# Optimization experiments

Measured on AMD Instinct MI355X. Metric: run time of the kernel, lower is better.

## Reference

```python
import jax, jax.numpy as jnp
import numpy as np

T = 4.0
B = 8192
C = 1024
N_CLASSES = 100

def setup_inputs() -> dict:
    key = jax.random.key(0)
    k1, k2 = jax.random.split(key)
    output = jax.random.normal(k1, (B, C), dtype=jnp.float32)
    target = jax.random.randint(k2, (B,), 0, N_CLASSES, dtype=jnp.int64)
    return {"output": output, "target": target}

def reference(output, target):
    # Faithful to the torch module:
    #   probs = softmax(logits / T) + 1e-8   (the label_inds masking is dead code,
    #   probs is immediately overwritten in the original)
    #   kl[i, j] = F.kl_div(probs[i], probs[j])  with default reduction='mean'
    #            = mean_c( probs[j] * (log(probs[j]) - probs[i]) )
    #   (note: torch kl_div treats its first arg as LOG-probs, but the original
    #    passes raw probs -- we reproduce that exactly)
    #   loss = sum over same-label pairs (i != j) of kl[i,j]**2, divided by batch.
    n_cats = output.shape[1]
    probs = jax.nn.softmax(output / T, axis=1) + 1e-8          # [B, C]
    # self-term t[j] = mean_c probs[j] * log probs[j]
    t = jnp.mean(probs * jnp.log(probs), axis=1)               # [B]
    # cross[i, j] = mean_c probs[j] * probs[i]  (single big GEMM)
    cross = (probs @ probs.T) / n_cats                         # [B, B]
    kl = t[None, :] - cross                                    # kl[i, j]
    labels = target
    same = labels[:, None] == labels[None, :]                  # [B, B]
    not_diag = ~jnp.eye(labels.shape[0], dtype=bool)
    mask = (same & not_diag).astype(kl.dtype)
    # |kl|^2 summed over valid pairs; groups of size 1 contribute no pairs,
    # matching the original's `continue`.
    loss = jnp.sum(mask * kl * kl) / labels.shape[0]
    return loss
```

## Files before the change

kernel.cpp:

```cpp
#include <hip/hip_runtime.h>

#define B_SZ 8192
#define C_SZ 1024
#define NCLS 100
#define INV_T 0.25f
#define MAX_ITEMS 65536
#define GRP 64
#define NCH 8

typedef unsigned int uint32;

using bf16x8 = __attribute__((ext_vector_type(8))) short;
using f32x16 = __attribute__((ext_vector_type(16))) float;

__device__ __forceinline__ unsigned short f2bf(float f) {
    uint32 u = __float_as_uint(f);
    u = u + 0x7fffu + ((u >> 16) & 1u);
    return (unsigned short)(u >> 16);
}

__device__ __forceinline__ void gload16_lds(const void* g, void* l) {
    __builtin_amdgcn_global_load_lds(
        (const __attribute__((address_space(1))) uint32*)g,
        (__attribute__((address_space(3))) uint32*)l, 16, 0, 0);
}

__global__ __launch_bounds__(256) void softmax_prep_kernel(
        const float* __restrict__ x, const int* __restrict__ target,
        uint32* __restrict__ probs_bf, float* __restrict__ t,
        int* __restrict__ counts, int* __restrict__ lists,
        int* __restrict__ items, int* __restrict__ nitems,
        float* __restrict__ accum, int* __restrict__ done_ctr) {
    int tid = threadIdx.x;

    if (blockIdx.x == 0) {
        __shared__ int cnt[NCLS];
        __shared__ int tbase[NCLS];
        if (tid < NCLS) cnt[tid] = 0;
        if (tid == 0) { accum[0] = 0.0f; done_ctr[0] = 0; }
        __syncthreads();
        #pragma unroll 4
        for (int i = 0; i < B_SZ / 256; i++) {
            int r = i * 256 + tid;
            int lbl = target[r];
            if (lbl < 0) lbl = 0;
            if (lbl >= NCLS) lbl = NCLS - 1;
            int slot = atomicAdd(&cnt[lbl], 1);
            lists[lbl * B_SZ + slot] = r;
        }
        __syncthreads();
        if (tid < NCLS) counts[tid] = cnt[tid];
        if (tid == 0) {
            int tot = 0;
            for (int k = 0; k < NCLS; k++) {
                int ng = (cnt[k] + GRP - 1) / GRP;
                tbase[k] = tot;
                tot += ng * ng;
            }
            nitems[0] = tot;
        }
        __syncthreads();
        if (tid < NCLS) {
            int ng = (cnt[tid] + GRP - 1) / GRP;
            int base = tbase[tid];
            int z = 0;
            for (int a = 0; a < ng; a++)
                for (int b = 0; b < ng; b++)
                    items[base + z++] = tid | (a << 8) | (b << 20);
        }
        return;
    }

    int row = blockIdx.x - 1;
    const float4* xr = (const float4*)(x + (size_t)row * C_SZ);
    float4 v = xr[tid];
    v.x *= INV_T; v.y *= INV_T; v.z *= INV_T; v.w *= INV_T;

    __shared__ float red[12];
    int wid = tid >> 6;

    float m = fmaxf(fmaxf(v.x, v.y), fmaxf(v.z, v.w));
    #pragma unroll
    for (int o = 32; o >= 1; o >>= 1) m = fmaxf(m, __shfl_xor(m, o, 64));
    if ((tid & 63) == 0) red[wid] = m;
    __syncthreads();
    m = fmaxf(fmaxf(red[0], red[1]), fmaxf(red[2], red[3]));

    float4 e;
    e.x = __expf(v.x - m); e.y = __expf(v.y - m);
    e.z = __expf(v.z - m); e.w = __expf(v.w - m);
    float s = (e.x + e.y) + (e.z + e.w);
    #pragma unroll
    for (int o = 32; o >= 1; o >>= 1) s += __shfl_xor(s, o, 64);
    if ((tid & 63) == 0) red[4 + wid] = s;
    __syncthreads();
    float Z = (red[4] + red[5]) + (red[6] + red[7]);
    float rZ = 1.0f / Z;

    float4 p;
    p.x = e.x * rZ + 1e-8f; p.y = e.y * rZ + 1e-8f;
    p.z = e.z * rZ + 1e-8f; p.w = e.w * rZ + 1e-8f;

    uint2 packed;
    packed.x = ((uint32)f2bf(p.y) << 16) | (uint32)f2bf(p.x);
    packed.y = ((uint32)f2bf(p.w) << 16) | (uint32)f2bf(p.z);
    ((uint2*)(probs_bf + (size_t)row * (C_SZ / 2)))[tid] = packed;

    float pl = p.x * __logf(p.x) + p.y * __logf(p.y) +
               p.z * __logf(p.z) + p.w * __logf(p.w);
    #pragma unroll
    for (int o = 32; o >= 1; o >>= 1) pl += __shfl_xor(pl, o, 64);
    if ((tid & 63) == 0) red[8 + wid] = pl;
    __syncthreads();
    if (tid == 0)
        t[row] = ((red[8] + red[9]) + (red[10] + red[11])) * (1.0f / C_SZ);
}

__global__ __launch_bounds__(256, 1) void pair_kernel(
        const char* __restrict__ probs, const float* __restrict__ t,
        const int* __restrict__ counts, const int* __restrict__ lists,
        const int* __restrict__ nitems, const int* __restrict__ items,
        float* __restrict__ accum, int* __restrict__ done_ctr,
        float* __restrict__ out) {
    __shared__ uint32 sA[2 * GRP * 64];
    __shared__ uint32 sB[2 * GRP * 64];
    __shared__ int s_ridA[GRP];
    __shared__ int s_ridB[GRP];
    __shared__ float s_tB[GRP];
    __shared__ float s_wsum[4];

    int tid = threadIdx.x;
    int wv = tid >> 6;
    int lane = tid & 63;
    int l = lane & 31;
    int h = lane >> 5;
    int NI = nitems[0];
    if (NI > MAX_ITEMS) NI = MAX_ITEMS;
    float lacc = 0.0f;

    for (int it = blockIdx.x; it < NI; it += (int)gridDim.x) {
        int pk = items[it];
        int k = pk & 255;
        if (k >= NCLS) continue;
        int gi = (pk >> 8) & 0xfff;
        int gj = pk >> 20;
        int m = counts[k];
        if (m < 1) continue;
        if (m > B_SZ) m = B_SZ;
        bool same = (gi == gj);

        __syncthreads();
        if (tid < GRP) {
            int which = gi * GRP + tid; if (which > m - 1) which = m - 1;
            s_ridA[tid] = lists[k * B_SZ + which] & (B_SZ - 1);
        } else if (tid < 2 * GRP) {
            int r = tid - GRP;
            int which = gj * GRP + r; if (which > m - 1) which = m - 1;
            int rid = lists[k * B_SZ + which] & (B_SZ - 1);
            s_ridB[r] = rid;
            s_tB[r] = t[rid];
        }
        __syncthreads();

        int rowsA = m - gi * GRP; if (rowsA > GRP) rowsA = GRP;
        int rowsB = m - gj * GRP; if (rowsB > GRP) rowsB = GRP;
        int ntA = (rowsA + 31) >> 5;
        int ntB = (rowsB + 31) >> 5;
        int npairs = ntA * ntB;
        int ti = wv / ntB;
        int tj = wv % ntB;

        #define STAGE(ch, bb)                                                     \
            _Pragma("unroll")                                                     \
            for (int rr = 0; rr < 8; rr++) {                                      \
                if (!(same && rr >= 4)) {                                         \
                    int slot = rr * 256 + tid;                                    \
                    int row = (slot >> 4) & 63;                                   \
                    int c16 = slot & 15;                                          \
                    int rid = (rr >= 4) ? s_ridB[row] : s_ridA[row];              \
                    const char* gp = probs + ((size_t)rid << 11) + ((ch) << 8) +  \
                                     ((c16 ^ (row & 7)) << 4);                    \
                    uint32* lp = ((rr >= 4) ? sB : sA) + (bb) * (GRP * 64) +      \
                                 (((rr & 3) * 256 + wv * 64) << 2);               \
                    gload16_lds(gp, lp);                                          \
                }                                                                 \
            }

        STAGE(0, 0);
        __syncthreads();

        f32x16 acc = {};
        int bb = 0;
        #pragma unroll 1
        for (int ch = 0; ch < NCH; ch++) {
            if (ch + 1 < NCH) STAGE(ch + 1, bb ^ 1);
            if (wv < npairs) {
                const uint32* pA = sA + bb * (GRP * 64);
                const uint32* pB = (same ? sA : sB) + bb * (GRP * 64);
                #pragma unroll
                for (int ks = 0; ks < 8; ks++) {
                    int ra = ti * 32 + l;
                    int ca = (ks * 2 + h) ^ (ra & 7);
                    bf16x8 av = *(const bf16x8*)(pA + ra * 64 + ca * 4);
                    int rb = tj * 32 + l;
                    int cb = (ks * 2 + h) ^ (rb & 7);
                    bf16x8 bv = *(const bf16x8*)(pB + rb * 64 + cb * 4);
                    acc = __builtin_amdgcn_mfma_f32_32x32x16_bf16(av, bv, acc, 0, 0, 0);
                }
            }
            __syncthreads();
            bb ^= 1;
        }
        #undef STAGE

        if (wv < npairs) {
            int jloc = tj * 32 + l;
            int jl = gj * GRP + jloc;
            bool jv = jl < m;
            float tjv = s_tB[jloc];
            float local = 0.0f;
            #pragma unroll
            for (int g = 0; g < 16; g++) {
                int rowloc = (g & 3) + 8 * (g >> 2) + 4 * h;
                int il = gi * GRP + ti * 32 + rowloc;
                if (jv && il < m && il != jl) {
                    float kl = tjv - acc[g] * (1.0f / C_SZ);
                    local += kl * kl;
                }
            }
            lacc += local;
        }
    }

    #pragma unroll
    for (int o = 32; o >= 1; o >>= 1) lacc += __shfl_xor(lacc, o, 64);
    __syncthreads();
    if (lane == 0) s_wsum[wv] = lacc;
    __syncthreads();
    if (tid == 0) {
        float tot = (s_wsum[0] + s_wsum[1]) + (s_wsum[2] + s_wsum[3]);
        atomicAdd(accum, tot);
        __threadfence();
        if (atomicAdd(done_ctr, 1) == (int)gridDim.x - 1) {
            __threadfence();
            out[0] = atomicAdd(accum, 0.0f) * (1.0f / B_SZ);
        }
    }
}

extern "C" void kernel_launch(void* const* d_in, const int* in_sizes, int n_in,
                              void* d_out, int out_size, void* d_ws, size_t ws_size,
                              hipStream_t stream) {
    const float* x = (const float*)d_in[0];
    const int* target = (const int*)d_in[1];
    float* out = (float*)d_out;

    char* ws = (char*)d_ws;
    uint32* probs_bf = (uint32*)ws;
    char* p = ws + (size_t)B_SZ * C_SZ * 2;
    float* t = (float*)p;            p += B_SZ * 4;
    int* counts = (int*)p;           p += 128 * 4;
    int* nitems = (int*)p;           p += 16;
    int* lists = (int*)p;            p += (size_t)NCLS * B_SZ * 4;
    int* items = (int*)p;            p += MAX_ITEMS * 4;
    float* accum = (float*)p;        p += 16;
    int* done_ctr = (int*)p;

    softmax_prep_kernel<<<B_SZ + 1, 256, 0, stream>>>(x, target, probs_bf, t,
                                                      counts, lists, items, nitems,
                                                      accum, done_ctr);
    pair_kernel<<<512, 256, 0, stream>>>((const char*)probs_bf, t, counts, lists,
                                         nitems, items, accum, done_ctr, out);
}
```

Baseline: 104.4 us.

## Exploit pair symmetry with 128-row groups and upper-triangular tile scheduling

Class groups grow to 128 rows, and only upper-triangular group pairs and tile pairs are scheduled. Off-diagonal tiles add both kl[i,j]^2 and kl[j,i]^2 from one GEMM result, using t of both the row and the column, which roughly halves the MFMA and load work. Blocks become 512 threads with 8 waves, each wave owning up to two 32x32 tiles. The loop uses explicit vmcnt waits and raw barriers for double-buffered global-to-LDS loads, and the grid shrinks to 128 blocks, which risks load imbalance and fewer waves resident across CUs.

```diff
diff --git a/kernel.cpp b/kernel.cpp
--- a/kernel.cpp
+++ b/kernel.cpp
@@ -5,8 +5,9 @@
 #define NCLS 100
 #define INV_T 0.25f
 #define MAX_ITEMS 65536
-#define GRP 64
 #define NCH 8
+#define GRP 128
+#define PAIR_GRID 128
 
 typedef unsigned int uint32;
 
@@ -55,7 +56,7 @@
             for (int k = 0; k < NCLS; k++) {
                 int ng = (cnt[k] + GRP - 1) / GRP;
                 tbase[k] = tot;
-                tot += ng * ng;
+                tot += ng * (ng + 1) / 2;
             }
             nitems[0] = tot;
         }
@@ -65,7 +66,7 @@
             int base = tbase[tid];
             int z = 0;
             for (int a = 0; a < ng; a++)
-                for (int b = 0; b < ng; b++)
+                for (int b = a; b < ng; b++)
                     items[base + z++] = tid | (a << 8) | (b << 20);
         }
         return;
@@ -116,24 +117,24 @@
         t[row] = ((red[8] + red[9]) + (red[10] + red[11])) * (1.0f / C_SZ);
 }
 
-__global__ __launch_bounds__(256, 1) void pair_kernel(
+__global__ __launch_bounds__(512, 2) void pair_kernel(
         const char* __restrict__ probs, const float* __restrict__ t,
         const int* __restrict__ counts, const int* __restrict__ lists,
         const int* __restrict__ nitems, const int* __restrict__ items,
         float* __restrict__ accum, int* __restrict__ done_ctr,
         float* __restrict__ out) {
-    __shared__ uint32 sA[2 * GRP * 64];
-    __shared__ uint32 sB[2 * GRP * 64];
+    __shared__ char sAB[2][2][32768];
     __shared__ int s_ridA[GRP];
     __shared__ int s_ridB[GRP];
+    __shared__ float s_tA[GRP];
     __shared__ float s_tB[GRP];
-    __shared__ float s_wsum[4];
+    __shared__ float s_wsum[8];
 
     int tid = threadIdx.x;
     int wv = tid >> 6;
-    int lane = tid & 63;
-    int l = lane & 31;
-    int h = lane >> 5;
+    int ln = tid & 63;
+    int l = ln & 31;
+    int h = ln >> 5;
     int NI = nitems[0];
     if (NI > MAX_ITEMS) NI = MAX_ITEMS;
     float lacc = 0.0f;
@@ -147,18 +148,20 @@
         int m = counts[k];
         if (m < 1) continue;
         if (m > B_SZ) m = B_SZ;
-        bool same = (gi == gj);
+        bool same_strip = (gi == gj);
 
         __syncthreads();
         if (tid < GRP) {
             int which = gi * GRP + tid; if (which > m - 1) which = m - 1;
-            s_ridA[tid] = lists[k * B_SZ + which] & (B_SZ - 1);
+            int r = lists[k * B_SZ + which] & (B_SZ - 1);
+            s_ridA[tid] = r;
+            s_tA[tid] = t[r];
         } else if (tid < 2 * GRP) {
-            int r = tid - GRP;
-            int which = gj * GRP + r; if (which > m - 1) which = m - 1;
-            int rid = lists[k * B_SZ + which] & (B_SZ - 1);
-            s_ridB[r] = rid;
-            s_tB[r] = t[rid];
+            int rb = tid - GRP;
+            int which = gj * GRP + rb; if (which > m - 1) which = m - 1;
+            int r = lists[k * B_SZ + which] & (B_SZ - 1);
+            s_ridB[rb] = r;
+            s_tB[rb] = t[r];
         }
         __syncthreads();
 
@@ -166,79 +169,145 @@
         int rowsB = m - gj * GRP; if (rowsB > GRP) rowsB = GRP;
         int ntA = (rowsA + 31) >> 5;
         int ntB = (rowsB + 31) >> 5;
-        int npairs = ntA * ntB;
-        int ti = wv / ntB;
-        int tj = wv % ntB;
-
-        #define STAGE(ch, bb)                                                     \
-            _Pragma("unroll")                                                     \
-            for (int rr = 0; rr < 8; rr++) {                                      \
-                if (!(same && rr >= 4)) {                                         \
-                    int slot = rr * 256 + tid;                                    \
-                    int row = (slot >> 4) & 63;                                   \
-                    int c16 = slot & 15;                                          \
-                    int rid = (rr >= 4) ? s_ridB[row] : s_ridA[row];              \
-                    const char* gp = probs + ((size_t)rid << 11) + ((ch) << 8) +  \
-                                     ((c16 ^ (row & 7)) << 4);                    \
-                    uint32* lp = ((rr >= 4) ? sB : sA) + (bb) * (GRP * 64) +      \
-                                 (((rr & 3) * 256 + wv * 64) << 2);               \
-                    gload16_lds(gp, lp);                                          \
-                }                                                                 \
-            }
-
-        STAGE(0, 0);
-        __syncthreads();
-
-        f32x16 acc = {};
-        int bb = 0;
-        #pragma unroll 1
-        for (int ch = 0; ch < NCH; ch++) {
-            if (ch + 1 < NCH) STAGE(ch + 1, bb ^ 1);
-            if (wv < npairs) {
-                const uint32* pA = sA + bb * (GRP * 64);
-                const uint32* pB = (same ? sA : sB) + bb * (GRP * 64);
+
+        int P = same_strip ? (ntA * (ntA + 1)) / 2 : ntA * ntB;
+        int tta[2], ttb[2], pv[2];
+        #pragma unroll
+        for (int slot = 0; slot < 2; slot++) {
+            int p = wv + slot * 8;
+            pv[slot] = (p < P);
+            int pp = pv[slot] ? p : 0;
+            int a = 0, b = 0;
+            if (same_strip) {
+                int rem = pp, len = ntA;
+                while (rem >= len) { rem -= len; a++; len--; }
+                b = a + rem;
+            } else {
+                a = pp / ntB; b = pp % ntB;
+            }
+            tta[slot] = a; ttb[slot] = b;
+        }
+
+        const char* gA[4];
+        const char* gB[4];
+        #pragma unroll
+        for (int s = 0; s < 4; s++) {
+            int row = s * 32 + wv * 4 + (ln >> 4);
+            int c16 = ln & 15;
+            int off = ((c16 ^ (row & 7)) << 4);
+            gA[s] = probs + ((size_t)s_ridA[row] << 11) + off;
+            gB[s] = probs + ((size_t)s_ridB[row] << 11) + off;
+        }
+
+        #define STAGE_A(ch, db)                                                \
+            _Pragma("unroll")                                                  \
+            for (int s = 0; s < 4; s++)                                        \
+                gload16_lds(gA[s] + ((ch) << 8), &sAB[db][0][s * 8192 + wv * 1024]);
+        #define STAGE_B(ch, db)                                                \
+            _Pragma("unroll")                                                  \
+            for (int s = 0; s < 4; s++)                                        \
+                gload16_lds(gB[s] + ((ch) << 8), &sAB[db][1][s * 8192 + wv * 1024]);
+
+        #define COMPUTE(db, bs)                                                \
+            { const char* bufA_ = &sAB[db][0][0];                              \
+              const char* bufB_ = &sAB[db][bs][0];                             \
+              _Pragma("unroll")                                                \
+              for (int slot = 0; slot < 2; slot++) {                           \
+                  if (pv[slot]) {                                              \
+                      _Pragma("unroll")                                        \
+                      for (int ks = 0; ks < 4; ks++) {                         \
+                          int ca = ((2 * ks + h) ^ (l & 7)) << 4;              \
+                          bf16x8 av = *(const bf16x8*)(bufA_ + (tta[slot] * 32 + l) * 256 + ca); \
+                          bf16x8 bv = *(const bf16x8*)(bufB_ + (ttb[slot] * 32 + l) * 256 + ca); \
+                          acc[slot] = __builtin_amdgcn_mfma_f32_32x32x16_bf16(av, bv, acc[slot], 0, 0, 0); \
+                      }                                                        \
+                  }                                                            \
+              } }
+
+        f32x16 acc[2] = {};
+        if (same_strip) {
+            STAGE_A(0, 0);
+            #pragma unroll 1
+            for (int ch = 0; ch < NCH; ch++) {
+                int db = ch & 1;
+                if (ch + 1 < NCH) {
+                    STAGE_A(ch + 1, db ^ 1);
+                    asm volatile("s_waitcnt vmcnt(4)" ::: "memory");
+                } else {
+                    asm volatile("s_waitcnt vmcnt(0)" ::: "memory");
+                }
+                __builtin_amdgcn_sched_barrier(0);
+                __builtin_amdgcn_s_barrier();
+                __builtin_amdgcn_sched_barrier(0);
+                COMPUTE(db, 0);
+                __builtin_amdgcn_sched_barrier(0);
+                __builtin_amdgcn_s_barrier();
+            }
+        } else {
+            STAGE_A(0, 0); STAGE_B(0, 0);
+            #pragma unroll 1
+            for (int ch = 0; ch < NCH; ch++) {
+                int db = ch & 1;
+                if (ch + 1 < NCH) {
+                    STAGE_A(ch + 1, db ^ 1); STAGE_B(ch + 1, db ^ 1);
+                    asm volatile("s_waitcnt vmcnt(8)" ::: "memory");
+                } else {
+                    asm volatile("s_waitcnt vmcnt(0)" ::: "memory");
+                }
+                __builtin_amdgcn_sched_barrier(0);
+                __builtin_amdgcn_s_barrier();
+                __builtin_amdgcn_sched_barrier(0);
+                COMPUTE(db, 1);
+                __builtin_amdgcn_sched_barrier(0);
+                __builtin_amdgcn_s_barrier();
+            }
+        }
+        #undef STAGE_A
+        #undef STAGE_B
+        #undef COMPUTE
+
+        float local = 0.0f;
+        #pragma unroll
+        for (int slot = 0; slot < 2; slot++) {
+            if (pv[slot]) {
+                bool dtile = same_strip && (tta[slot] == ttb[slot]);
+                int jloc = ttb[slot] * 32 + l;
+                int jl = gj * GRP + jloc;
+                bool jv = jl < m;
+                float tcol = s_tB[jloc];
                 #pragma unroll
-                for (int ks = 0; ks < 8; ks++) {
-                    int ra = ti * 32 + l;
-                    int ca = (ks * 2 + h) ^ (ra & 7);
-                    bf16x8 av = *(const bf16x8*)(pA + ra * 64 + ca * 4);
-                    int rb = tj * 32 + l;
-                    int cb = (ks * 2 + h) ^ (rb & 7);
-                    bf16x8 bv = *(const bf16x8*)(pB + rb * 64 + cb * 4);
-                    acc = __builtin_amdgcn_mfma_f32_32x32x16_bf16(av, bv, acc, 0, 0, 0);
+                for (int g = 0; g < 16; g++) {
+                    int rowloc = (g & 3) + 8 * (g >> 2) + 4 * h;
+                    int iloc = tta[slot] * 32 + rowloc;
+                    int il = gi * GRP + iloc;
+                    bool iv = il < m;
+                    float c = acc[slot][g] * (1.0f / C_SZ);
+                    if (dtile) {
+                        if (iv && jv && il != jl) {
+                            float kl = tcol - c; local += kl * kl;
+                        }
+                    } else {
+                        if (iv && jv) {
+                            float k1 = tcol - c;
+                            float k2 = s_tA[iloc] - c;
+                            local += k1 * k1 + k2 * k2;
+                        }
+                    }
                 }
             }
-            __syncthreads();
-            bb ^= 1;
-        }
-        #undef STAGE
-
-        if (wv < npairs) {
-            int jloc = tj * 32 + l;
-            int jl = gj * GRP + jloc;
-            bool jv = jl < m;
-            float tjv = s_tB[jloc];
-            float local = 0.0f;
-            #pragma unroll
-            for (int g = 0; g < 16; g++) {
-                int rowloc = (g & 3) + 8 * (g >> 2) + 4 * h;
-                int il = gi * GRP + ti * 32 + rowloc;
-                if (jv && il < m && il != jl) {
-                    float kl = tjv - acc[g] * (1.0f / C_SZ);
-                    local += kl * kl;
-                }
-            }
-            lacc += local;
-        }
+        }
+        lacc += local;
     }
 
     #pragma unroll
     for (int o = 32; o >= 1; o >>= 1) lacc += __shfl_xor(lacc, o, 64);
     __syncthreads();
-    if (lane == 0) s_wsum[wv] = lacc;
+    if (ln == 0) s_wsum[wv] = lacc;
     __syncthreads();
     if (tid == 0) {
-        float tot = (s_wsum[0] + s_wsum[1]) + (s_wsum[2] + s_wsum[3]);
+        float tot = 0.0f;
+        #pragma unroll
+        for (int w = 0; w < 8; w++) tot += s_wsum[w];
         atomicAdd(accum, tot);
         __threadfence();
         if (atomicAdd(done_ctr, 1) == (int)gridDim.x - 1) {
@@ -269,6 +338,7 @@
     softmax_prep_kernel<<<B_SZ + 1, 256, 0, stream>>>(x, target, probs_bf, t,
                                                       counts, lists, items, nitems,
                                                       accum, done_ctr);
-    pair_kernel<<<512, 256, 0, stream>>>((const char*)probs_bf, t, counts, lists,
-                                         nitems, items, accum, done_ctr, out);
-}
+    pair_kernel<<<PAIR_GRID, 512, 0, stream>>>((const char*)probs_bf, t, counts,
+                                               lists, nitems, items, accum,
+                                               done_ctr, out);
+}
```

Measured after the change: 97.02 us. -7.1%, faster.
